# Kernel optimization log

Hardware: AMD Instinct MI355X
Metric: run time of the kernel (lower is better)

The kernel has to match this reference:

```python
import jax, jax.numpy as jnp
import numpy as np

EPS = 2.220446049250313e-16  # sys.float_info.epsilon, matches CoCosNet feature_normalize

def feature_normalize(x):
    return x / (jnp.linalg.norm(x, axis=1, keepdims=True) + EPS)

def conv1x1(x, w, b):  # w: (out, in)
    return jnp.einsum('bchw,oc->bohw', x, w) + b[None, :, None, None]

def conv3x3(x, w, b):  # w: (out, in, 3, 3), SAME padding, stride 1
    y = jax.lax.conv_general_dilated(x, w, (1, 1), 'SAME',
                                     dimension_numbers=('NCHW', 'OIHW', 'NCHW'))
    return y + b[None, :, None, None]

@jax.custom_vjp
def sign_sig(x):
    return (x > 0).astype(x.dtype)

def _ss_fwd(x):
    return (x > 0).astype(x.dtype), jax.nn.sigmoid(x)

def _ss_bwd(s, g):
    return (g * s * (1.0 - s),)

sign_sig.defvjp(_ss_fwd, _ss_bwd)

def pono(x, eps=1e-5):  # PositionalNorm2d: normalize over channel dim
    m = jnp.mean(x, axis=1, keepdims=True)
    v = jnp.var(x, axis=1, keepdims=True)
    return (x - m) * jax.lax.rsqrt(v + eps)

def instance_norm(x, eps=1e-5):  # param-free, over spatial dims
    m = jnp.mean(x, axis=(2, 3), keepdims=True)
    v = jnp.var(x, axis=(2, 3), keepdims=True)
    return (x - m) * jax.lax.rsqrt(v + eps)

def setup_inputs() -> dict:
    B, CV, CPOS, H, W = 2, 256, 64, 64, 64
    CQK, DP, IC, NH = CV + CPOS, 64, 3, 128
    key = jax.random.key(0)
    ks = jax.random.split(key, 24)
    n = lambda i, s: jax.random.normal(ks[i], s, jnp.float32)
    w = lambda i, s: n(i, s) * 0.02
    z = lambda s: jnp.zeros(s, jnp.float32)
    return dict(
        q=n(0, (B, CV, H, W)), k=n(1, (B, CV, H, W)), v=n(2, (B, CV, H, W)),
        pos=n(3, (1, CPOS, H, W)),
        seg_map=jax.random.uniform(ks[4], (B, IC, H, W), jnp.float32),
        v2=n(5, (B, CV, H, W)),
        f_w=w(6, (CQK, CQK)), f_b=z(CQK),
        g_w=w(7, (CQK, CQK)), g_b=z(CQK),
        h_w=w(8, (CV, CV)), h_b=z(CV),
        fp_w=w(9, (DP, CQK)), fp_b=z(DP),
        gp_w=w(10, (DP, CQK)), gp_b=z(DP),
        sp_s_w=w(11, (NH, IC, 3, 3)), sp_s_b=z(NH),
        sp_g_w=w(12, (CV, NH, 3, 3)), sp_g_b=z(CV),
        sp_b_w=w(13, (CV, NH, 3, 3)), sp_b_b=z(CV),
        r1_w=w(14, (CV, CV, 3, 3)), r1_b=z(CV),
        r2_w=w(15, (CV, CV, 3, 3)), r2_b=z(CV),
    )

def reference(q, k, v, pos, seg_map, v2,
              f_w, f_b, g_w, g_b, h_w, h_b, fp_w, fp_b, gp_w, gp_b,
              sp_s_w, sp_s_b, sp_g_w, sp_g_b, sp_b_w, sp_b_b,
              r1_w, r1_b, r2_w, r2_b):
    b, cv, h, w = q.shape
    posb = jnp.broadcast_to(pos, (b,) + pos.shape[1:])
    query = jnp.concatenate([feature_normalize(q), posb], axis=1)
    keyt = jnp.concatenate([feature_normalize(k), posb], axis=1)
    qf = conv1x1(query, f_w, f_b)
    kf = conv1x1(keyt, g_w, g_b)
    vh = conv1x1(v, h_w, h_b)
    qp = conv1x1(query, fp_w, fp_b)
    kp = conv1x1(keyt, gp_w, gp_b)
    cqk = qf.shape[1]
    n = h * w
    Q = qf.reshape(b, cqk, n).transpose(0, 2, 1)          # (b, N, c_qk)
    K = kf.reshape(b, cqk, n)                             # (b, c_qk, N)
    V = vh.reshape(b, cv, n).transpose(0, 2, 1)           # (b, N, c_v)
    Qp = qp.reshape(b, -1, n).transpose(0, 2, 1)
    Kp = kp.reshape(b, -1, n)
    mask = sign_sig(jnp.einsum('bnc,bcm->bnm', Qp, Kp) / Kp.shape[1])
    cor = jnp.einsum('bnc,bcm->bnm', Q, K) / jnp.sqrt(jnp.float32(cqk))
    attn = jax.nn.softmax(cor, axis=-1)
    masked = attn * mask
    out = jnp.einsum('bnm,bmc->bnc', masked, V).transpose(0, 2, 1).reshape(b, cv, h, w)
    conf = masked.sum(-1).reshape(b, 1, h, w)
    V2 = v2.reshape(b, -1, n).transpose(0, 2, 1)
    attn2 = jax.nn.softmax(jnp.where(mask > 0, jnp.float32(-10000.0), cor), axis=-1)
    out2 = jnp.einsum('bnm,bmc->bnc', attn2, V2).transpose(0, 2, 1).reshape(b, -1, h, w)
    # SPADE(q, seg_map)
    actv = jax.nn.relu(conv3x3(seg_map, sp_s_w, sp_s_b))
    spade = instance_norm(q) * (1.0 + conv3x3(actv, sp_g_w, sp_g_b)) + conv3x3(actv, sp_b_w, sp_b_b)
    y = pono(out + (1.0 - conf) * spade + q)
    res = y + conv3x3(jax.nn.relu(conv3x3(y, r1_w, r1_b)), r2_w, r2_b)
    return (res, out2, cor)
```

## Files before the change

### kernel.cpp

```cpp
#include <hip/hip_runtime.h>
#include <stdint.h>


#define DEV static __device__ __forceinline__

typedef short short8 __attribute__((ext_vector_type(8)));
typedef float floatx4 __attribute__((ext_vector_type(4)));

DEV float bf2f(unsigned short b) { return __uint_as_float(((unsigned int)b) << 16); }
DEV unsigned short f2bf(float f) {
  unsigned int u = __float_as_uint(f);
  u += 0x7FFFu + ((u >> 16) & 1u);
  return (unsigned short)(u >> 16);
}
DEV float bfround(float f) { return bf2f(f2bf(f)); }

__global__ __launch_bounds__(256)
void cvt_f2b(const float* __restrict__ in, unsigned short* __restrict__ out, int n)
{
  int i = blockIdx.x * 256 + threadIdx.x;
  if (i < n) out[i] = f2bf(in[i]);
}

__global__ __launch_bounds__(256)
void prep_w9(const float* __restrict__ w, unsigned short* __restrict__ w9,
             int CO, int CI)
{
  int i = blockIdx.x * 256 + threadIdx.x;
  int tot = CO * CI * 9;
  if (i >= tot) return;
  int s = i % 9, rest = i / 9;
  int ci = rest % CI, o = rest / CI;
  w9[(long long)o * 9 * CI + s * CI + ci] = f2bf(w[i]);
}

__global__ __launch_bounds__(256)
void colnorm(const float* __restrict__ x, float* __restrict__ rnorm)
{
  int b = blockIdx.y, t = threadIdx.x;
  int n = (blockIdx.x << 5) + (t & 31);
  int cg = t >> 5;
  const float* base = x + ((long long)b << 20) + n;
  float s = 0.f;
#pragma unroll
  for (int c8 = 0; c8 < 32; c8++) {
    float v = base[((long long)(cg * 32 + c8)) << 12];
    s += v * v;
  }
  __shared__ float red[256];
  red[t] = s; __syncthreads();
  for (int st = 128; st >= 32; st >>= 1) {
    if (t < st) red[t] += red[t + st];
    __syncthreads();
  }
  if (t < 32)
    rnorm[(b << 12) + n] = 1.f / (sqrtf(red[t]) + 2.2204460492503131e-16f);
}

__global__ __launch_bounds__(256)
void build_qk3(const float* __restrict__ x, const float* __restrict__ pos,
               const float* __restrict__ rnorm, unsigned short* __restrict__ qt)
{
  __shared__ float tile[64][65];
  int b = blockIdx.z, by = blockIdx.y;
  int n0 = blockIdx.x << 6;
  int tx = threadIdx.x & 63, tg = threadIdx.x >> 6;
  const float* ib;
  int c0;
  if (by < 4) { ib = x + ((long long)b << 20) + ((long long)(by << 6) << 12); c0 = by << 6; }
  else        { ib = pos; c0 = 256; }
#pragma unroll
  for (int i = 0; i < 16; i++) {
    int r = tg * 16 + i;
    tile[r][tx] = ib[((long long)r << 12) + n0 + tx];
  }
  __syncthreads();
#pragma unroll
  for (int i = 0; i < 16; i++) {
    int r = tg * 16 + i;
    float sc = (by < 4) ? rnorm[(b << 12) + n0 + r] : 1.f;
    qt[((long long)(b * 4096 + n0 + r)) * 320 + c0 + tx] = f2bf(tile[tx][r] * sc);
  }
}

__global__ __launch_bounds__(256)
void transpose_c(const float* __restrict__ in, unsigned short* __restrict__ out, int C)
{
  __shared__ float tile[64][65];
  int b = blockIdx.z;
  int c0 = blockIdx.y << 6;
  int n0 = blockIdx.x << 6;
  const float* ib = in + (long long)b * C * 4096;
  unsigned short* ob = out + (long long)b * C * 4096;
  int tx = threadIdx.x & 63, tg = threadIdx.x >> 6;
#pragma unroll
  for (int i = 0; i < 16; i++) {
    int r = tg * 16 + i;
    tile[r][tx] = ib[((long long)(c0 + r) << 12) + n0 + tx];
  }
  __syncthreads();
#pragma unroll
  for (int i = 0; i < 16; i++) {
    int r = tg * 16 + i;
    ob[(long long)(n0 + r) * C + c0 + tx] = f2bf(tile[tx][r]);
  }
}

__global__ __launch_bounds__(256)
void gemm_bt(const unsigned short* __restrict__ A, long long sAb, int lda,
             const unsigned short* __restrict__ Bt, long long sBb, int ldb,
             int Ncols, int K, float alpha,
             const float* __restrict__ bias, int biasMode,
             unsigned short* __restrict__ Cb, long long sCbb, int ldcb,
             float* __restrict__ Cf, long long sCfb, int ldcf,
             unsigned short* __restrict__ Cm)
{
  __shared__ unsigned short As[128][40];
  __shared__ unsigned short Bs[128][40];
  int bz = blockIdx.z;
  const unsigned short* Ab = A + bz * sAb;
  const unsigned short* Bb = Bt + bz * sBb;
  int m0 = blockIdx.y << 7, n0 = blockIdx.x << 7;
  int t = threadIdx.x;
  int lane = t & 63, wave = t >> 6, quad = lane >> 4, l16 = lane & 15;
  int wm = (wave >> 1) << 6, wn = (wave & 1) << 6;

  floatx4 acc[4][4] = {};

  for (int k0 = 0; k0 < K; k0 += 32) {
#pragma unroll
    for (int s = 0; s < 2; s++) {
      int idx = t + (s << 8);
      int row = idx >> 2, ch = (idx & 3) << 3;
      short8 av = *(const short8*)(Ab + (long long)(m0 + row) * lda + k0 + ch);
      *(short8*)&As[row][ch] = av;
      short8 bv = {};
      if (n0 + row < Ncols) bv = *(const short8*)(Bb + (long long)(n0 + row) * ldb + k0 + ch);
      *(short8*)&Bs[row][ch] = bv;
    }
    __syncthreads();
    short8 af[4], bfv[4];
#pragma unroll
    for (int i = 0; i < 4; i++) af[i] = *(const short8*)&As[wm + (i << 4) + l16][quad << 3];
#pragma unroll
    for (int j = 0; j < 4; j++) bfv[j] = *(const short8*)&Bs[wn + (j << 4) + l16][quad << 3];
#pragma unroll
    for (int i = 0; i < 4; i++)
#pragma unroll
      for (int j = 0; j < 4; j++)
        acc[i][j] = __builtin_amdgcn_mfma_f32_16x16x32_bf16(af[i], bfv[j], acc[i][j], 0, 0, 0);
    __syncthreads();
  }

#pragma unroll
  for (int j = 0; j < 4; j++) {
    int col = n0 + wn + (j << 4) + l16;
    if (col >= Ncols) continue;
    float bcol = (biasMode == 1) ? bias[col] : 0.f;
#pragma unroll
    for (int i = 0; i < 4; i++) {
#pragma unroll
      for (int r = 0; r < 4; r++) {
        int row = m0 + wm + (i << 4) + (quad << 2) + r;
        float vv = acc[i][j][r] * alpha + bcol;
        if (biasMode == 2) vv += bias[row];
        if (Cb) Cb[bz * sCbb + (long long)row * ldcb + col] = f2bf(vv);
        if (Cf) Cf[bz * sCfb + (long long)row * ldcf + col] = bfround(vv);
        if (Cm) {
          unsigned long long bal = __ballot(vv > 0.f);
          if (l16 == 0)
            Cm[(long long)bz * 4096 * 256 + (long long)row * 256 + ((n0 + wn + (j << 4)) >> 4)]
              = (unsigned short)(bal >> (quad << 4));
        }
      }
    }
  }
}

__global__ __launch_bounds__(256)
void gemm_conv2(const unsigned short* __restrict__ Xt, int CI,
                const unsigned short* __restrict__ W9, int CO,
                const float* __restrict__ bias,
                unsigned short* __restrict__ Cb, int relu,
                float* __restrict__ Cf, const float* __restrict__ addT, int rnd,
                float* __restrict__ Cf2)
{
  __shared__ unsigned short As[64][40];
  __shared__ unsigned short Bs[128][40];
  int bz = blockIdx.z;
  const unsigned short* Xb = Xt + (long long)bz * 4096 * CI;
  int m0 = blockIdx.y << 6, n0 = blockIdx.x << 7;
  int t = threadIdx.x;
  int lane = t & 63, wave = t >> 6, quad = lane >> 4, l16 = lane & 15;
  int wm = (wave >> 1) << 5, wn = (wave & 1) << 6;
  int K9 = 9 * CI;

  floatx4 acc[2][4] = {};

  for (int tap = 0; tap < 9; ++tap) {
    int dy = tap / 3 - 1, dx = tap % 3 - 1;
    int off = dy * 64 + dx;
    for (int kc = 0; kc < CI; kc += 32) {
      {
        int row = t >> 2, ch = (t & 3) << 3;
        int p = m0 + row;
        int y = (p >> 6) + dy, x = (p & 63) + dx;
        short8 av = {};
        if ((unsigned)y < 64u && (unsigned)x < 64u)
          av = *(const short8*)(Xb + (long long)(p + off) * CI + kc + ch);
        *(short8*)&As[row][ch] = av;
      }
#pragma unroll
      for (int s = 0; s < 2; s++) {
        int idx = t + (s << 8);
        int row = idx >> 2, ch = (idx & 3) << 3;
        short8 bv = *(const short8*)(W9 + (long long)(n0 + row) * K9 + tap * CI + kc + ch);
        *(short8*)&Bs[row][ch] = bv;
      }
      __syncthreads();
      short8 af[2], bfv[4];
#pragma unroll
      for (int i = 0; i < 2; i++) af[i] = *(const short8*)&As[wm + (i << 4) + l16][quad << 3];
#pragma unroll
      for (int j = 0; j < 4; j++) bfv[j] = *(const short8*)&Bs[wn + (j << 4) + l16][quad << 3];
#pragma unroll
      for (int i = 0; i < 2; i++)
#pragma unroll
        for (int j = 0; j < 4; j++)
          acc[i][j] = __builtin_amdgcn_mfma_f32_16x16x32_bf16(af[i], bfv[j], acc[i][j], 0, 0, 0);
      __syncthreads();
    }
  }

#pragma unroll
  for (int j = 0; j < 4; j++) {
    int col = n0 + wn + (j << 4) + l16;
    float bcol = bias[col];
#pragma unroll
    for (int i = 0; i < 2; i++) {
#pragma unroll
      for (int r = 0; r < 4; r++) {
        int row = m0 + wm + (i << 4) + (quad << 2) + r;
        float vv = acc[i][j][r] + bcol;
        if (relu) vv = fmaxf(vv, 0.f);
        if (Cb) Cb[((long long)bz * 4096 + row) * CO + col] = f2bf(vv);
        if (Cf) {
          long long oi = (((long long)bz * 256 + (col & 255)) << 12) + row;
          float ov = vv;
          if (addT) ov += addT[oi];
          float* dst = (col < 256) ? Cf : Cf2;
          dst[oi] = rnd ? bfround(ov) : ov;
        }
      }
    }
  }
}

__global__ __launch_bounds__(256)
void conv3x3(const float* __restrict__ inF,
             const float* __restrict__ wgt, const float* __restrict__ bias,
             int CI, int CO, const float* __restrict__ addF,
             float* __restrict__ outF, int relu, int rnd)
{
  __shared__ float wsm[2304];
  int b = blockIdx.z, o = blockIdx.y, t = threadIdx.x;
  for (int i = t; i < CI * 9; i += 256) wsm[i] = wgt[(long long)o * CI * 9 + i];
  __syncthreads();
  int x = t & 63, y = (blockIdx.x << 2) + (t >> 6);
  bool ym = y > 0, yp = y < 63, xm = x > 0, xp = x < 63;
  int p = y * 64 + x;
  long long ibase = ((long long)b * CI) << 12;
  float acc = bias[o];
  for (int ci = 0; ci < CI; ci++) {
    const float* wp = &wsm[ci * 9];
    long long ib = ibase + ((long long)ci << 12) + p;
    float v00 = (ym && xm) ? inF[ib - 65] : 0.f;
    float v01 = ym ? inF[ib - 64] : 0.f;
    float v02 = (ym && xp) ? inF[ib - 63] : 0.f;
    float v10 = xm ? inF[ib - 1] : 0.f;
    float v11 = inF[ib];
    float v12 = xp ? inF[ib + 1] : 0.f;
    float v20 = (yp && xm) ? inF[ib + 63] : 0.f;
    float v21 = yp ? inF[ib + 64] : 0.f;
    float v22 = (yp && xp) ? inF[ib + 65] : 0.f;
    acc += v00 * wp[0] + v01 * wp[1] + v02 * wp[2]
         + v10 * wp[3] + v11 * wp[4] + v12 * wp[5]
         + v20 * wp[6] + v21 * wp[7] + v22 * wp[8];
  }
  if (relu) acc = fmaxf(acc, 0.f);
  long long oidx = (((long long)(b * CO + o)) << 12) + p;
  if (addF) acc += addF[oidx];
  outF[oidx] = rnd ? bfround(acc) : acc;
}

__global__ __launch_bounds__(256)
void stats_rows(const float* __restrict__ corF,
                const unsigned char* __restrict__ mbits,
                float4* __restrict__ statA, float* __restrict__ confF)
{
  long long row = blockIdx.x;
  const float4* cr = (const float4*)(corF + (row << 12));
  const unsigned char* mr = mbits + row * 512;
  int t = threadIdx.x;

  float lg[16]; unsigned int mk[16];
#pragma unroll
  for (int i = 0; i < 4; i++) {
    float4 cc = cr[i * 256 + t];
    unsigned char mb = mr[(i * 256 + t) >> 1];
    int sh = (t & 1) << 2;
    lg[4 * i + 0] = cc.x; lg[4 * i + 1] = cc.y;
    lg[4 * i + 2] = cc.z; lg[4 * i + 3] = cc.w;
#pragma unroll
    for (int j = 0; j < 4; j++) mk[4 * i + j] = (mb >> (sh + j)) & 1u;
  }
  float m1 = -3.0e38f, m2 = -3.0e38f; int cnt = 0;
#pragma unroll
  for (int e = 0; e < 16; e++) {
    m1 = fmaxf(m1, lg[e]);
    if (!mk[e]) m2 = fmaxf(m2, lg[e]);
    cnt += (int)mk[e];
  }
  __shared__ float4 red4[256];
  red4[t] = make_float4(m1, m2, 0.f, 0.f); __syncthreads();
  for (int s = 128; s > 0; s >>= 1) {
    if (t < s) {
      red4[t].x = fmaxf(red4[t].x, red4[t + s].x);
      red4[t].y = fmaxf(red4[t].y, red4[t + s].y);
    }
    __syncthreads();
  }
  float rmax1 = red4[0].x;
  float rmax2 = fmaxf(red4[0].y, -10000.f);
  __syncthreads();

  float s1 = 0.f, cn = 0.f, s2 = 0.f;
#pragma unroll
  for (int e = 0; e < 16; e++) {
    float ex = __expf(fminf(lg[e] - rmax1, 0.f));
    s1 += ex;
    if (mk[e]) cn += ex;
    else s2 += __expf(fminf(lg[e] - rmax2, 0.f));
  }
  red4[t] = make_float4(s1, cn, s2, (float)cnt); __syncthreads();
  for (int s = 128; s > 0; s >>= 1) {
    if (t < s) {
      red4[t].x += red4[t + s].x; red4[t].y += red4[t + s].y;
      red4[t].z += red4[t + s].z; red4[t].w += red4[t + s].w;
    }
    __syncthreads();
  }
  if (t == 0) {
    float4 r = red4[0];
    float sum2 = r.z + r.w * __expf(fminf(-10000.f - rmax2, 0.f));
    statA[row] = make_float4(rmax1, 1.f / fmaxf(r.x, 1e-30f),
                             rmax2, 1.f / fmaxf(sum2, 1e-30f));
    confF[row] = r.y / fmaxf(r.x, 1e-30f);
  }
}

__global__ __launch_bounds__(256, 2)
void gemm_pv4(const float* __restrict__ corF,
              const unsigned char* __restrict__ mbits,
              const float4* __restrict__ statA,
              const unsigned short* __restrict__ Bt0,
              const unsigned short* __restrict__ Bt1,
              float* __restrict__ Cf0, float* __restrict__ Cf1)
{
  __shared__ unsigned short As[32][40];
  __shared__ unsigned short Bs[256][40];
  __shared__ float2 sstat[32];
  int bz = blockIdx.y & 1, mode = blockIdx.y >> 1;
  const float* corb = corF + (long long)bz * 4096 * 4096;
  const unsigned char* mbb = mbits + (long long)bz * 4096 * 512;
  const unsigned short* Bb = (mode ? Bt1 : Bt0) + (long long)bz * 256 * 4096;
  int m0 = blockIdx.x << 5;
  int t = threadIdx.x;
  int lane = t & 63, wave = t >> 6, quad = lane >> 4, l16 = lane & 15;
  int wn = wave << 6;
  const float L2E = 1.44269504088896340736f;

  if (t < 32) {
    float4 s = statA[(long long)bz * 4096 + m0 + t];
    float rm = mode ? s.z : s.x, iv = mode ? s.w : s.y;
    sstat[t] = make_float2(-rm * L2E, iv);
  }
  __syncthreads();

  int rA = t >> 3, cA = (t & 7) << 2;
  int rB = t >> 2, cB = (t & 3) << 3;
  float nrmL = sstat[rA].x;
  float mvr = exp2f(-10000.f * L2E + nrmL);

  floatx4 acc[2][4] = {};

  const float* cpb = corb + (long long)(m0 + rA) * 4096 + cA;
  const unsigned char* mbp = mbb + (long long)(m0 + rA) * 512;
  const unsigned short* pbb = Bb + (long long)rB * 4096 + cB;

  float4 pa; short8 pb[4]; unsigned int pmk;
  auto issue = [&](int kk) {
    pa = *(const float4*)(cpb + kk);
    pmk = (unsigned int)(mbp[(kk + cA) >> 3] >> (cA & 7)) & 0xFu;
#pragma unroll
    for (int j = 0; j < 4; j++)
      pb[j] = *(const short8*)(pbb + (long long)(j << 6) * 4096 + kk);
  };

  issue(0);
  for (int k0 = 0; k0 < 4096; k0 += 32) {
    {
      float cs[4] = {pa.x, pa.y, pa.z, pa.w};
      float vs[4];
#pragma unroll
      for (int j = 0; j < 4; j++) {
        float e = exp2f(fmaf(cs[j], L2E, nrmL));
        bool mk = (pmk >> j) & 1u;
        vs[j] = mode ? (mk ? mvr : e) : (mk ? e : 0.f);
      }
      unsigned int u01, u23;
      asm("v_cvt_pk_bf16_f32 %0, %1, %2" : "=v"(u01) : "v"(vs[0]), "v"(vs[1]));
      asm("v_cvt_pk_bf16_f32 %0, %1, %2" : "=v"(u23) : "v"(vs[2]), "v"(vs[3]));
      *(unsigned int*)&As[rA][cA] = u01;
      *(unsigned int*)&As[rA][cA + 2] = u23;
#pragma unroll
      for (int j = 0; j < 4; j++)
        *(short8*)&Bs[rB + (j << 6)][cB] = pb[j];
    }
    __syncthreads();
    if (k0 + 32 < 4096) issue(k0 + 32);
    short8 af[2], bfv[4];
#pragma unroll
    for (int i = 0; i < 2; i++) af[i] = *(const short8*)&As[(i << 4) + l16][quad << 3];
#pragma unroll
    for (int j = 0; j < 4; j++) bfv[j] = *(const short8*)&Bs[wn + (j << 4) + l16][quad << 3];
#pragma unroll
    for (int i = 0; i < 2; i++)
#pragma unroll
      for (int j = 0; j < 4; j++)
        acc[i][j] = __builtin_amdgcn_mfma_f32_16x16x32_bf16(af[i], bfv[j], acc[i][j], 0, 0, 0);
    __syncthreads();
  }

#pragma unroll
  for (int j = 0; j < 4; j++) {
    int col = wn + (j << 4) + l16;
#pragma unroll
    for (int i = 0; i < 2; i++) {
#pragma unroll
      for (int r = 0; r < 4; r++) {
        int lrow = (i << 4) + (quad << 2) + r;
        int row = m0 + lrow;
        float vv = bfround(acc[i][j][r] * sstat[lrow].y);
        if (mode) Cf1[(long long)bz * 256 * 4096 + (long long)col * 4096 + row] = vv;
        else      Cf0[(long long)bz * 4096 * 256 + (long long)row * 256 + col] = vv;
      }
    }
  }
}

__global__ __launch_bounds__(256)
void inorm_stats(const float* __restrict__ q, float* __restrict__ mu, float* __restrict__ rs)
{
  int c = blockIdx.x, b = blockIdx.y, t = threadIdx.x;
  const float* base = q + ((long long)(b * 256 + c) << 12);
  float s = 0.f, s2 = 0.f;
  for (int i = t; i < 4096; i += 256) { float v = base[i]; s += v; s2 += v * v; }
  __shared__ float r1[256], r2[256];
  r1[t] = s; r2[t] = s2; __syncthreads();
  for (int st = 128; st > 0; st >>= 1) {
    if (t < st) { r1[t] += r1[t + st]; r2[t] += r2[t + st]; }
    __syncthreads();
  }
  if (t == 0) {
    float m = r1[0] * (1.f / 4096.f);
    float var = fmaxf(r2[0] * (1.f / 4096.f) - m * m, 0.f);
    mu[b * 256 + c] = m;
    rs[b * 256 + c] = rsqrtf(var + 1e-5f);
  }
}

__global__ __launch_bounds__(256)
void pono_y(const float* __restrict__ outF, const float* __restrict__ confF,
            const float* __restrict__ gF, const float* __restrict__ bF,
            const float* __restrict__ q, const float* __restrict__ mu,
            const float* __restrict__ rs, float* __restrict__ yF,
            unsigned short* __restrict__ yT)
{
  int n = blockIdx.x, b = blockIdx.y, c = threadIdx.x;
  long long cn = ((long long)(b * 256 + c) << 12) + n;
  float qv = q[cn];
  float sp = (qv - mu[b * 256 + c]) * rs[b * 256 + c] * (1.f + gF[cn]) + bF[cn];
  float cf = confF[b * 4096 + n];
  float tv = outF[((long long)(b * 4096 + n) << 8) + c] + (1.f - cf) * sp + qv;
  __shared__ float red[256];
  red[c] = tv; __syncthreads();
  for (int s = 128; s > 0; s >>= 1) { if (c < s) red[c] += red[c + s]; __syncthreads(); }
  float m = red[0] * (1.f / 256.f); __syncthreads();
  float d = tv - m;
  red[c] = d * d; __syncthreads();
  for (int s = 128; s > 0; s >>= 1) { if (c < s) red[c] += red[c + s]; __syncthreads(); }
  float var = fmaxf(red[0] * (1.f / 256.f), 0.f);
  float yv = d * rsqrtf(var + 1e-5f);
  yF[cn] = yv;
  yT[((long long)(b * 4096 + n) << 8) + c] = f2bf(yv);
}


extern "C" void kernel_launch(void* const* d_in, const int* in_sizes, int n_in,
                              void* d_out, int out_size, void* d_ws, size_t ws_size,
                              hipStream_t stream)
{
  (void)in_sizes; (void)n_in; (void)out_size; (void)ws_size;
  const int B = 2, CV = 256, CQK = 320, DP = 64, N = 4096, NH = 128, IC = 3;
  const float INV_SQRT_CQK = 0.05590169943749474241f;

  const float* q    = (const float*)d_in[0];
  const float* k    = (const float*)d_in[1];
  const float* v    = (const float*)d_in[2];
  const float* pos  = (const float*)d_in[3];
  const float* seg  = (const float*)d_in[4];
  const float* v2   = (const float*)d_in[5];
  const float* f_w  = (const float*)d_in[6];
  const float* f_b  = (const float*)d_in[7];
  const float* g_w  = (const float*)d_in[8];
  const float* g_b  = (const float*)d_in[9];
  const float* h_w  = (const float*)d_in[10];
  const float* h_b  = (const float*)d_in[11];
  const float* fp_w = (const float*)d_in[12];
  const float* fp_b = (const float*)d_in[13];
  const float* gp_w = (const float*)d_in[14];
  const float* gp_b = (const float*)d_in[15];
  const float* sp_s_w = (const float*)d_in[16];
  const float* sp_s_b = (const float*)d_in[17];
  const float* sp_g_w = (const float*)d_in[18];
  const float* sp_g_b = (const float*)d_in[19];
  const float* sp_b_w = (const float*)d_in[20];
  const float* sp_b_b = (const float*)d_in[21];
  const float* r1_w = (const float*)d_in[22];
  const float* r1_b = (const float*)d_in[23];
  const float* r2_w = (const float*)d_in[24];
  const float* r2_b = (const float*)d_in[25];

  float* res_o  = (float*)d_out;
  float* out2_o = res_o + (long long)B * CV * N;
  float* cor_o  = res_o + 2ll * B * CV * N;

  unsigned short* query_t = (unsigned short*)cor_o;
  unsigned short* keyt_t  = query_t + (long long)B * N * CQK;
  float*          outBuf  = res_o;

  char* wp_ = (char*)d_ws;
  auto take = [&](size_t bytes) -> void* {
    void* r = wp_; wp_ += (bytes + 255) & ~(size_t)255; return r;
  };
  unsigned short* v_t     = (unsigned short*)take((size_t)B * N * CV * 2);
  unsigned short* qf_t    = (unsigned short*)take((size_t)B * N * CQK * 2);
  unsigned short* kf_t    = (unsigned short*)take((size_t)B * N * CQK * 2);
  unsigned short* qp_t    = (unsigned short*)take((size_t)B * N * DP * 2);
  unsigned short* kp_t    = (unsigned short*)take((size_t)B * N * DP * 2);
  unsigned short* vh      = (unsigned short*)take((size_t)B * CV * N * 2);
  unsigned short* v2b     = (unsigned short*)take((size_t)B * CV * N * 2);
  unsigned short* fwB     = (unsigned short*)take((size_t)CQK * CQK * 2);
  unsigned short* gwB     = (unsigned short*)take((size_t)CQK * CQK * 2);
  unsigned short* fpwB    = (unsigned short*)take((size_t)DP * CQK * 2);
  unsigned short* gpwB    = (unsigned short*)take((size_t)DP * CQK * 2);
  unsigned short* hwB     = (unsigned short*)take((size_t)CV * CV * 2);
  unsigned short* maskB16 = (unsigned short*)take((size_t)B * N * 256 * 2);
  float4*         statA   = (float4*)take((size_t)B * N * 16);
  float*          confF   = (float*)take((size_t)B * N * 4);
  float*          muF     = (float*)take((size_t)B * CV * 4);
  float*          rsF     = (float*)take((size_t)B * CV * 4);
  float*          rnormQ  = (float*)take((size_t)B * N * 4);
  float*          rnormK  = (float*)take((size_t)B * N * 4);
  float*          actv    = (float*)take((size_t)B * NH * N * 4);
  float*          gC      = (float*)take((size_t)B * CV * N * 4);
  float*          bC      = (float*)take((size_t)B * CV * N * 4);
  float*          yF      = (float*)take((size_t)B * CV * N * 4);
  unsigned short* spW9    = (unsigned short*)take((size_t)2 * CV * 9 * NH * 2);
  unsigned short* r1W9    = (unsigned short*)take((size_t)CV * 9 * CV * 2);
  unsigned short* r2W9    = (unsigned short*)take((size_t)CV * 9 * CV * 2);
  float*          spBias  = (float*)take((size_t)2 * CV * 4);
  unsigned short* yT      = qf_t;
  unsigned short* a1T     = kf_t;
  unsigned short* actvT   = v_t;

  dim3 blk(256);
  auto cvt = [&](const float* in, unsigned short* out, int n) {
    cvt_f2b<<<dim3((n + 255) / 256), blk, 0, stream>>>(in, out, n);
  };
  auto prepw = [&](const float* w, unsigned short* w9, int CO, int CI) {
    prep_w9<<<dim3((CO * CI * 9 + 255) / 256), blk, 0, stream>>>(w, w9, CO, CI);
  };
  auto gemm = [&](const unsigned short* A, long long sAb, int lda,
                  const unsigned short* Bt, long long sBb, int ldb,
                  int M, int Nc, int K, float alpha,
                  const float* bias, int biasMode,
                  unsigned short* Cb, long long sCbb, int ldcb,
                  float* Cf, long long sCfb, int ldcf,
                  unsigned short* Cm) {
    dim3 grid((Nc + 127) / 128, M / 128, B);
    gemm_bt<<<grid, blk, 0, stream>>>(A, sAb, lda, Bt, sBb, ldb, Nc, K, alpha,
                                      bias, biasMode, Cb, sCbb, ldcb,
                                      Cf, sCfb, ldcf, Cm);
  };
  auto conv = [&](const unsigned short* Xt, int CI, const unsigned short* W9,
                  int CO, const float* bias, unsigned short* Cb, int relu,
                  float* Cf, const float* addT, int rnd, float* Cf2) {
    gemm_conv2<<<dim3(CO / 128, N / 64, B), blk, 0, stream>>>(
        Xt, CI, W9, CO, bias, Cb, relu, Cf, addT, rnd, Cf2);
  };

  cvt(f_w, fwB, CQK * CQK);
  cvt(g_w, gwB, CQK * CQK);
  cvt(fp_w, fpwB, DP * CQK);
  cvt(gp_w, gpwB, DP * CQK);
  cvt(h_w, hwB, CV * CV);
  cvt(v2, v2b, B * CV * N);
  prepw(sp_g_w, spW9, CV, NH);
  prepw(sp_b_w, spW9 + (size_t)CV * 9 * NH, CV, NH);
  prepw(r1_w, r1W9, CV, CV);
  prepw(r2_w, r2W9, CV, CV);
  hipMemcpyAsync(spBias, sp_g_b, CV * sizeof(float), hipMemcpyDeviceToDevice, stream);
  hipMemcpyAsync(spBias + CV, sp_b_b, CV * sizeof(float), hipMemcpyDeviceToDevice, stream);

  colnorm<<<dim3(128, B), blk, 0, stream>>>(q, rnormQ);
  colnorm<<<dim3(128, B), blk, 0, stream>>>(k, rnormK);
  build_qk3<<<dim3(64, 5, B), blk, 0, stream>>>(q, pos, rnormQ, query_t);
  build_qk3<<<dim3(64, 5, B), blk, 0, stream>>>(k, pos, rnormK, keyt_t);
  transpose_c<<<dim3(64, 4, B), blk, 0, stream>>>(v, v_t, CV);

  gemm(query_t, (long long)N * CQK, CQK, fwB, 0, CQK, N, CQK, CQK, 1.f, f_b, 1,
       qf_t, (long long)N * CQK, CQK, nullptr, 0, 0, nullptr);
  gemm(keyt_t, (long long)N * CQK, CQK, gwB, 0, CQK, N, CQK, CQK, 1.f, g_b, 1,
       kf_t, (long long)N * CQK, CQK, nullptr, 0, 0, nullptr);
  gemm(query_t, (long long)N * CQK, CQK, fpwB, 0, CQK, N, DP, CQK, 1.f, fp_b, 1,
       qp_t, (long long)N * DP, DP, nullptr, 0, 0, nullptr);
  gemm(keyt_t, (long long)N * CQK, CQK, gpwB, 0, CQK, N, DP, CQK, 1.f, gp_b, 1,
       kp_t, (long long)N * DP, DP, nullptr, 0, 0, nullptr);
  gemm(hwB, 0, CV, v_t, (long long)N * CV, CV, CV, N, CV, 1.f, h_b, 2,
       vh, (long long)CV * N, N, nullptr, 0, 0, nullptr);

  gemm(qf_t, (long long)N * CQK, CQK, kf_t, (long long)N * CQK, CQK, N, N, CQK,
       INV_SQRT_CQK, nullptr, 0, nullptr, 0, 0,
       cor_o, (long long)N * N, N, nullptr);
  gemm(qp_t, (long long)N * DP, DP, kp_t, (long long)N * DP, DP, N, N, DP, 1.f,
       nullptr, 0, nullptr, 0, 0, nullptr, 0, 0, maskB16);

  stats_rows<<<dim3(B * N), blk, 0, stream>>>(cor_o, (const unsigned char*)maskB16,
                                              statA, confF);
  gemm_pv4<<<dim3(128, 2 * B), blk, 0, stream>>>(
      cor_o, (const unsigned char*)maskB16, statA, vh, v2b, outBuf, out2_o);

  inorm_stats<<<dim3(CV, B), blk, 0, stream>>>(q, muF, rsF);
  conv3x3<<<dim3(16, NH, B), blk, 0, stream>>>(seg, sp_s_w, sp_s_b, IC, NH, nullptr, actv, 1, 0);
  transpose_c<<<dim3(64, 2, B), blk, 0, stream>>>(actv, actvT, NH);
  conv(actvT, NH, spW9, 2 * CV, spBias, nullptr, 0, gC, nullptr, 0, bC);
  pono_y<<<dim3(N, B), blk, 0, stream>>>(outBuf, confF, gC, bC, q, muF, rsF, yF, yT);
  conv(yT, CV, r1W9, CV, r1_b, a1T, 1, nullptr, nullptr, 0, nullptr);
  conv(a1T, CV, r2W9, CV, r2_b, nullptr, 0, res_o, yF, 1, nullptr);
}
```

Baseline: 738.1 us.

## Fuse Q/K projection GEMMs and double K-tile depth in PV GEMM

The f/fp and g/gp 1x1 projection weights are concatenated so that each of query and key needs one GEMM producing a combined 384-wide output, replacing four launches with two. The cor and mask GEMMs then read strided slices of these combined buffers. The PV kernel now processes a 64-wide K tile per iteration with 8-element A loads and two MFMA sub-steps, halving the number of barrier-separated iterations. The cost is more registers and LDS per block, which could lower occupancy, and strided access with ld=384 in the attention GEMMs.

```diff
diff --git a/kernel.cpp b/kernel.cpp
--- a/kernel.cpp
+++ b/kernel.cpp
@@ -360,15 +360,15 @@
 }
 
 __global__ __launch_bounds__(256, 2)
-void gemm_pv4(const float* __restrict__ corF,
-              const unsigned char* __restrict__ mbits,
-              const float4* __restrict__ statA,
-              const unsigned short* __restrict__ Bt0,
-              const unsigned short* __restrict__ Bt1,
-              float* __restrict__ Cf0, float* __restrict__ Cf1)
-{
-  __shared__ unsigned short As[32][40];
-  __shared__ unsigned short Bs[256][40];
+void gemm_pv4b(const float* __restrict__ corF,
+               const unsigned char* __restrict__ mbits,
+               const float4* __restrict__ statA,
+               const unsigned short* __restrict__ Bt0,
+               const unsigned short* __restrict__ Bt1,
+               float* __restrict__ Cf0, float* __restrict__ Cf1)
+{
+  __shared__ unsigned short As[32][72];
+  __shared__ unsigned short Bs[256][72];
   __shared__ float2 sstat[32];
   int bz = blockIdx.y & 1, mode = blockIdx.y >> 1;
   const float* corb = corF + (long long)bz * 4096 * 4096;
@@ -387,7 +387,7 @@
   }
   __syncthreads();
 
-  int rA = t >> 3, cA = (t & 7) << 2;
+  int rA = t >> 3, cA = (t & 7) << 3;
   int rB = t >> 2, cB = (t & 3) << 3;
   float nrmL = sstat[rA].x;
   float mvr = exp2f(-10000.f * L2E + nrmL);
@@ -398,47 +398,58 @@
   const unsigned char* mbp = mbb + (long long)(m0 + rA) * 512;
   const unsigned short* pbb = Bb + (long long)rB * 4096 + cB;
 
-  float4 pa; short8 pb[4]; unsigned int pmk;
+  float4 pa0, pa1; short8 pb[8]; unsigned int pmk;
   auto issue = [&](int kk) {
-    pa = *(const float4*)(cpb + kk);
-    pmk = (unsigned int)(mbp[(kk + cA) >> 3] >> (cA & 7)) & 0xFu;
+    pa0 = *(const float4*)(cpb + kk);
+    pa1 = *(const float4*)(cpb + kk + 4);
+    pmk = (unsigned int)mbp[(kk + cA) >> 3];
 #pragma unroll
     for (int j = 0; j < 4; j++)
-      pb[j] = *(const short8*)(pbb + (long long)(j << 6) * 4096 + kk);
+#pragma unroll
+      for (int h = 0; h < 2; h++)
+        pb[j * 2 + h] = *(const short8*)(pbb + (long long)(j << 6) * 4096 + kk + (h << 5));
   };
 
   issue(0);
-  for (int k0 = 0; k0 < 4096; k0 += 32) {
+  for (int k0 = 0; k0 < 4096; k0 += 64) {
     {
-      float cs[4] = {pa.x, pa.y, pa.z, pa.w};
-      float vs[4];
-#pragma unroll
-      for (int j = 0; j < 4; j++) {
+      float cs[8] = {pa0.x, pa0.y, pa0.z, pa0.w, pa1.x, pa1.y, pa1.z, pa1.w};
+      float vs[8];
+#pragma unroll
+      for (int j = 0; j < 8; j++) {
         float e = exp2f(fmaf(cs[j], L2E, nrmL));
         bool mk = (pmk >> j) & 1u;
         vs[j] = mode ? (mk ? mvr : e) : (mk ? e : 0.f);
       }
-      unsigned int u01, u23;
-      asm("v_cvt_pk_bf16_f32 %0, %1, %2" : "=v"(u01) : "v"(vs[0]), "v"(vs[1]));
-      asm("v_cvt_pk_bf16_f32 %0, %1, %2" : "=v"(u23) : "v"(vs[2]), "v"(vs[3]));
-      *(unsigned int*)&As[rA][cA] = u01;
-      *(unsigned int*)&As[rA][cA + 2] = u23;
+      union { unsigned int u4[4]; short8 s8; } pk;
+      asm("v_cvt_pk_bf16_f32 %0, %1, %2" : "=v"(pk.u4[0]) : "v"(vs[0]), "v"(vs[1]));
+      asm("v_cvt_pk_bf16_f32 %0, %1, %2" : "=v"(pk.u4[1]) : "v"(vs[2]), "v"(vs[3]));
+      asm("v_cvt_pk_bf16_f32 %0, %1, %2" : "=v"(pk.u4[2]) : "v"(vs[4]), "v"(vs[5]));
+      asm("v_cvt_pk_bf16_f32 %0, %1, %2" : "=v"(pk.u4[3]) : "v"(vs[6]), "v"(vs[7]));
+      *(short8*)&As[rA][cA] = pk.s8;
 #pragma unroll
       for (int j = 0; j < 4; j++)
-        *(short8*)&Bs[rB + (j << 6)][cB] = pb[j];
-    }
-    __syncthreads();
-    if (k0 + 32 < 4096) issue(k0 + 32);
-    short8 af[2], bfv[4];
-#pragma unroll
-    for (int i = 0; i < 2; i++) af[i] = *(const short8*)&As[(i << 4) + l16][quad << 3];
-#pragma unroll
-    for (int j = 0; j < 4; j++) bfv[j] = *(const short8*)&Bs[wn + (j << 4) + l16][quad << 3];
-#pragma unroll
-    for (int i = 0; i < 2; i++)
+#pragma unroll
+        for (int h = 0; h < 2; h++)
+          *(short8*)&Bs[rB + (j << 6)][cB + (h << 5)] = pb[j * 2 + h];
+    }
+    __syncthreads();
+    if (k0 + 64 < 4096) issue(k0 + 64);
+#pragma unroll
+    for (int ks = 0; ks < 2; ks++) {
+      short8 af[2], bfv[4];
+#pragma unroll
+      for (int i = 0; i < 2; i++)
+        af[i] = *(const short8*)&As[(i << 4) + l16][(quad << 3) + (ks << 5)];
 #pragma unroll
       for (int j = 0; j < 4; j++)
-        acc[i][j] = __builtin_amdgcn_mfma_f32_16x16x32_bf16(af[i], bfv[j], acc[i][j], 0, 0, 0);
+        bfv[j] = *(const short8*)&Bs[wn + (j << 4) + l16][(quad << 3) + (ks << 5)];
+#pragma unroll
+      for (int i = 0; i < 2; i++)
+#pragma unroll
+        for (int j = 0; j < 4; j++)
+          acc[i][j] = __builtin_amdgcn_mfma_f32_16x16x32_bf16(af[i], bfv[j], acc[i][j], 0, 0, 0);
+    }
     __syncthreads();
   }
 
@@ -513,6 +524,7 @@
 {
   (void)in_sizes; (void)n_in; (void)out_size; (void)ws_size;
   const int B = 2, CV = 256, CQK = 320, DP = 64, N = 4096, NH = 128, IC = 3;
+  const int CQD = CQK + DP;
   const float INV_SQRT_CQK = 0.05590169943749474241f;
 
   const float* q    = (const float*)d_in[0];
@@ -555,16 +567,12 @@
     void* r = wp_; wp_ += (bytes + 255) & ~(size_t)255; return r;
   };
   unsigned short* v_t     = (unsigned short*)take((size_t)B * N * CV * 2);
-  unsigned short* qf_t    = (unsigned short*)take((size_t)B * N * CQK * 2);
-  unsigned short* kf_t    = (unsigned short*)take((size_t)B * N * CQK * 2);
-  unsigned short* qp_t    = (unsigned short*)take((size_t)B * N * DP * 2);
-  unsigned short* kp_t    = (unsigned short*)take((size_t)B * N * DP * 2);
+  unsigned short* qfq_t   = (unsigned short*)take((size_t)B * N * CQD * 2);
+  unsigned short* kfq_t   = (unsigned short*)take((size_t)B * N * CQD * 2);
   unsigned short* vh      = (unsigned short*)take((size_t)B * CV * N * 2);
   unsigned short* v2b     = (unsigned short*)take((size_t)B * CV * N * 2);
-  unsigned short* fwB     = (unsigned short*)take((size_t)CQK * CQK * 2);
-  unsigned short* gwB     = (unsigned short*)take((size_t)CQK * CQK * 2);
-  unsigned short* fpwB    = (unsigned short*)take((size_t)DP * CQK * 2);
-  unsigned short* gpwB    = (unsigned short*)take((size_t)DP * CQK * 2);
+  unsigned short* fqwB    = (unsigned short*)take((size_t)CQD * CQK * 2);
+  unsigned short* gqwB    = (unsigned short*)take((size_t)CQD * CQK * 2);
   unsigned short* hwB     = (unsigned short*)take((size_t)CV * CV * 2);
   unsigned short* maskB16 = (unsigned short*)take((size_t)B * N * 256 * 2);
   float4*         statA   = (float4*)take((size_t)B * N * 16);
@@ -581,8 +589,10 @@
   unsigned short* r1W9    = (unsigned short*)take((size_t)CV * 9 * CV * 2);
   unsigned short* r2W9    = (unsigned short*)take((size_t)CV * 9 * CV * 2);
   float*          spBias  = (float*)take((size_t)2 * CV * 4);
-  unsigned short* yT      = qf_t;
-  unsigned short* a1T     = kf_t;
+  float*          fqBias  = (float*)take((size_t)CQD * 4);
+  float*          gqBias  = (float*)take((size_t)CQD * 4);
+  unsigned short* yT      = qfq_t;
+  unsigned short* a1T     = kfq_t;
   unsigned short* actvT   = v_t;
 
   dim3 blk(256);
@@ -611,10 +621,10 @@
         Xt, CI, W9, CO, bias, Cb, relu, Cf, addT, rnd, Cf2);
   };
 
-  cvt(f_w, fwB, CQK * CQK);
-  cvt(g_w, gwB, CQK * CQK);
-  cvt(fp_w, fpwB, DP * CQK);
-  cvt(gp_w, gpwB, DP * CQK);
+  cvt(f_w, fqwB, CQK * CQK);
+  cvt(fp_w, fqwB + (size_t)CQK * CQK, DP * CQK);
+  cvt(g_w, gqwB, CQK * CQK);
+  cvt(gp_w, gqwB + (size_t)CQK * CQK, DP * CQK);
   cvt(h_w, hwB, CV * CV);
   cvt(v2, v2b, B * CV * N);
   prepw(sp_g_w, spW9, CV, NH);
@@ -623,6 +633,10 @@
   prepw(r2_w, r2W9, CV, CV);
   hipMemcpyAsync(spBias, sp_g_b, CV * sizeof(float), hipMemcpyDeviceToDevice, stream);
   hipMemcpyAsync(spBias + CV, sp_b_b, CV * sizeof(float), hipMemcpyDeviceToDevice, stream);
+  hipMemcpyAsync(fqBias, f_b, CQK * sizeof(float), hipMemcpyDeviceToDevice, stream);
+  hipMemcpyAsync(fqBias + CQK, fp_b, DP * sizeof(float), hipMemcpyDeviceToDevice, stream);
+  hipMemcpyAsync(gqBias, g_b, CQK * sizeof(float), hipMemcpyDeviceToDevice, stream);
+  hipMemcpyAsync(gqBias + CQK, gp_b, DP * sizeof(float), hipMemcpyDeviceToDevice, stream);
 
   colnorm<<<dim3(128, B), blk, 0, stream>>>(q, rnormQ);
   colnorm<<<dim3(128, B), blk, 0, stream>>>(k, rnormK);
@@ -630,26 +644,23 @@
   build_qk3<<<dim3(64, 5, B), blk, 0, stream>>>(k, pos, rnormK, keyt_t);
   transpose_c<<<dim3(64, 4, B), blk, 0, stream>>>(v, v_t, CV);
 
-  gemm(query_t, (long long)N * CQK, CQK, fwB, 0, CQK, N, CQK, CQK, 1.f, f_b, 1,
-       qf_t, (long long)N * CQK, CQK, nullptr, 0, 0, nullptr);
-  gemm(keyt_t, (long long)N * CQK, CQK, gwB, 0, CQK, N, CQK, CQK, 1.f, g_b, 1,
-       kf_t, (long long)N * CQK, CQK, nullptr, 0, 0, nullptr);
-  gemm(query_t, (long long)N * CQK, CQK, fpwB, 0, CQK, N, DP, CQK, 1.f, fp_b, 1,
-       qp_t, (long long)N * DP, DP, nullptr, 0, 0, nullptr);
-  gemm(keyt_t, (long long)N * CQK, CQK, gpwB, 0, CQK, N, DP, CQK, 1.f, gp_b, 1,
-       kp_t, (long long)N * DP, DP, nullptr, 0, 0, nullptr);
+  gemm(query_t, (long long)N * CQK, CQK, fqwB, 0, CQK, N, CQD, CQK, 1.f, fqBias, 1,
+       qfq_t, (long long)N * CQD, CQD, nullptr, 0, 0, nullptr);
+  gemm(keyt_t, (long long)N * CQK, CQK, gqwB, 0, CQK, N, CQD, CQK, 1.f, gqBias, 1,
+       kfq_t, (long long)N * CQD, CQD, nullptr, 0, 0, nullptr);
   gemm(hwB, 0, CV, v_t, (long long)N * CV, CV, CV, N, CV, 1.f, h_b, 2,
        vh, (long long)CV * N, N, nullptr, 0, 0, nullptr);
 
-  gemm(qf_t, (long long)N * CQK, CQK, kf_t, (long long)N * CQK, CQK, N, N, CQK,
+  gemm(qfq_t, (long long)N * CQD, CQD, kfq_t, (long long)N * CQD, CQD, N, N, CQK,
        INV_SQRT_CQK, nullptr, 0, nullptr, 0, 0,
        cor_o, (long long)N * N, N, nullptr);
-  gemm(qp_t, (long long)N * DP, DP, kp_t, (long long)N * DP, DP, N, N, DP, 1.f,
+  gemm(qfq_t + CQK, (long long)N * CQD, CQD, kfq_t + CQK, (long long)N * CQD, CQD,
+       N, N, DP, 1.f,
        nullptr, 0, nullptr, 0, 0, nullptr, 0, 0, maskB16);
 
   stats_rows<<<dim3(B * N), blk, 0, stream>>>(cor_o, (const unsigned char*)maskB16,
                                               statA, confF);
-  gemm_pv4<<<dim3(128, 2 * B), blk, 0, stream>>>(
+  gemm_pv4b<<<dim3(128, 2 * B), blk, 0, stream>>>(
       cor_o, (const unsigned char*)maskB16, statA, vh, v2b, outBuf, out2_o);
 
   inorm_stats<<<dim3(CV, B), blk, 0, stream>>>(q, muF, rsF);
```

Result: faster. 697.0 us (-5.6%).
